# Performance work log

Hardware: AMD Instinct MI355X
Metric: run time of the kernel (lower is better)

Reference implementation:

```python
import jax, jax.numpy as jnp
import numpy as np

N_MODULES = 8
AG_HIDDEN = 512
N_HID = 512
OUT_SIZE = 10
BATCH = 8192


def _state_mask(n_modules, n0, n1):
    # torch: eye(M).repeat_interleave(n0, 0).repeat_interleave(n1, 1)
    m = jnp.eye(n_modules, dtype=jnp.float32)
    return jnp.repeat(jnp.repeat(m, n0, axis=0), n1, axis=1)


def setup_inputs() -> dict:
    key = jax.random.key(0)
    ks = jax.random.split(key, 5)
    d_in = N_MODULES * AG_HIDDEN
    d_hid = N_MODULES * N_HID
    d_out = N_MODULES * OUT_SIZE
    s1 = 1.0 / np.sqrt(d_in)
    s2 = 1.0 / np.sqrt(d_hid)
    return {
        "x": jax.random.normal(ks[0], (BATCH, d_in), jnp.float32),
        "W1": jax.random.uniform(ks[1], (d_hid, d_in), jnp.float32, -s1, s1),
        "b1": jax.random.uniform(ks[2], (d_hid,), jnp.float32, -s1, s1),
        "W2": jax.random.uniform(ks[3], (d_out, d_hid), jnp.float32, -s2, s2),
        "b2": jax.random.uniform(ks[4], (d_out,), jnp.float32, -s2, s2),
    }


def reference(x, W1, b1, W2, b2):
    # block-diagonal masks (intra-module connectivity only)
    mask1 = _state_mask(N_MODULES, N_HID, AG_HIDDEN)   # [d_hid, d_in]
    mask2 = _state_mask(N_MODULES, OUT_SIZE, N_HID)    # [d_out, d_hid]
    h = jax.nn.relu(x @ (W1 * mask1).T + b1)           # [B, d_hid]
    y = h @ (W2 * mask2).T + b2                        # [B, d_out]
    # split(OUT_SIZE, -1) then stack on dim 1 == reshape to [B, n_modules, OUT_SIZE]
    return y.reshape(y.shape[0], N_MODULES, OUT_SIZE)
```

## Files before the change

### kernel.cpp

```cpp
#include <hip/hip_runtime.h>


#define NMOD 8
#define DIM 512
#define OSZ 10
#define BATCH 8192
#define D_IN 4096
#define D_OUT 80
#define BM 128
#define BK 32

typedef __attribute__((ext_vector_type(8))) short short8;
typedef __attribute__((ext_vector_type(4))) float float4v;

__device__ __forceinline__ unsigned short f2bf(float f) {
    unsigned int u = __builtin_bit_cast(unsigned int, f);
    u += 0x7fffu + ((u >> 16) & 1u);
    return (unsigned short)(u >> 16);
}

__device__ __forceinline__ short8 cvt8(float4 a, float4 b) {
    short8 r;
    r[0] = (short)f2bf(a.x); r[1] = (short)f2bf(a.y); r[2] = (short)f2bf(a.z); r[3] = (short)f2bf(a.w);
    r[4] = (short)f2bf(b.x); r[5] = (short)f2bf(b.y); r[6] = (short)f2bf(b.z); r[7] = (short)f2bf(b.w);
    return r;
}

__global__ void cvt_w_kernel(const float* __restrict__ W1, ushort* __restrict__ w1b) {
    int j = blockIdx.x * 256 + threadIdx.x;
    int mm = j >> 16, rem = j & 65535, r = rem >> 7, c4 = rem & 127;
    float4 v = *(const float4*)(W1 + (size_t)(mm * DIM + r) * D_IN + mm * DIM + c4 * 4);
    *(ushort4*)(w1b + (size_t)mm * DIM * DIM + r * DIM + c4 * 4) =
        make_ushort4(f2bf(v.x), f2bf(v.y), f2bf(v.z), f2bf(v.w));
}

template <bool WPRE>
__global__ __launch_bounds__(512, 2)
void fused_kernel(const float* __restrict__ x, const float* __restrict__ W1,
                  const ushort* __restrict__ w1b, const float* __restrict__ b1,
                  const float* __restrict__ W2, const float* __restrict__ b2,
                  float* __restrict__ out) {
    __shared__ ushort smem[40960];
    ushort* ldsA  = smem;
    ushort* ldsB  = smem + 4096;
    ushort* ldsH  = smem;
    ushort* ldsW2 = smem + 32768;

    const int tid  = threadIdx.x;
    const int wave = tid >> 6;
    const int lane = tid & 63;
    const int r16  = lane & 15;
    const int kq   = lane >> 4;

    const int bid     = blockIdx.x;
    const int m       = bid & 7;
    const int rowBase = (bid >> 3) * BM;

    {
        const int row = tid >> 5;
        const int col = (tid & 31) * 16;
        short8 v0 = {0, 0, 0, 0, 0, 0, 0, 0};
        short8 v1 = {0, 0, 0, 0, 0, 0, 0, 0};
        if (row < OSZ) {
            const float* s = W2 + (size_t)(m * OSZ + row) * D_IN + m * DIM + col;
            v0 = cvt8(*(const float4*)s, *(const float4*)(s + 4));
            v1 = cvt8(*(const float4*)(s + 8), *(const float4*)(s + 12));
        }
        const int sw = (row & 7) << 3;
        *(short8*)(ldsW2 + row * DIM + (col ^ sw))       = v0;
        *(short8*)(ldsW2 + row * DIM + ((col + 8) ^ sw)) = v1;
    }

    const float*  xsrc = x + (size_t)rowBase * D_IN + m * DIM;
    const ushort* w1m  = w1b + (size_t)m * DIM * DIM;
    const float*  w1f  = W1 + (size_t)(m * DIM) * D_IN + m * DIM;

    float4v acc[8][4];
#pragma unroll
    for (int i = 0; i < 8; i++)
#pragma unroll
        for (int j = 0; j < 4; j++) acc[i][j] = (float4v){0.f, 0.f, 0.f, 0.f};

    const int arow = tid >> 2;
    const int akc  = tid & 3;

    for (int kk = 0; kk < DIM / BK; kk++) {
        const int k0 = kk * BK;
        {
            const float* s = xsrc + (size_t)arow * D_IN + k0 + akc * 8;
            *(short8*)(ldsA + arow * BK + akc * 8) = cvt8(*(const float4*)s, *(const float4*)(s + 4));
        }
        if (WPRE) {
#pragma unroll
            for (int r = 0; r < 4; r++) {
                short8 v = *(const short8*)(w1m + (size_t)(r * 128 + arow) * DIM + k0 + akc * 8);
                *(short8*)(ldsB + (r * 128 + arow) * BK + akc * 8) = v;
            }
        } else {
#pragma unroll
            for (int r = 0; r < 4; r++) {
                const float* s = w1f + (size_t)(r * 128 + arow) * D_IN + k0 + akc * 8;
                *(short8*)(ldsB + (r * 128 + arow) * BK + akc * 8) =
                    cvt8(*(const float4*)s, *(const float4*)(s + 4));
            }
        }
        __syncthreads();

        short8 aF[8], bF[4];
#pragma unroll
        for (int mt = 0; mt < 8; mt++)
            aF[mt] = *(const short8*)(ldsA + (mt * 16 + r16) * BK + kq * 8);
#pragma unroll
        for (int nt = 0; nt < 4; nt++)
            bF[nt] = *(const short8*)(ldsB + (wave * 64 + nt * 16 + r16) * BK + kq * 8);
#pragma unroll
        for (int mt = 0; mt < 8; mt++)
#pragma unroll
            for (int nt = 0; nt < 4; nt++)
                acc[mt][nt] = __builtin_amdgcn_mfma_f32_16x16x32_bf16(aF[mt], bF[nt], acc[mt][nt], 0, 0, 0);
        __syncthreads();
    }

    float b1v[4];
#pragma unroll
    for (int nt = 0; nt < 4; nt++)
        b1v[nt] = b1[m * DIM + wave * 64 + nt * 16 + r16];

    for (int hh = 0; hh < 2; hh++) {
#pragma unroll
        for (int mt2 = 0; mt2 < 4; mt2++) {
            const int mt = hh * 4 + mt2;
#pragma unroll
            for (int nt = 0; nt < 4; nt++) {
#pragma unroll
                for (int reg = 0; reg < 4; reg++) {
                    float v = acc[mt][nt][reg] + b1v[nt];
                    v = v > 0.f ? v : 0.f;
                    const int lr  = mt2 * 16 + kq * 4 + reg;
                    const int col = wave * 64 + nt * 16 + r16;
                    ldsH[lr * DIM + (col ^ ((lr & 7) << 3))] = f2bf(v);
                }
            }
        }
        __syncthreads();

        if (wave < 4) {
            float4v acc2 = (float4v){0.f, 0.f, 0.f, 0.f};
            const int hrow = wave * 16 + r16;
            const int hsw  = (hrow & 7) << 3;
            const int wsw  = (r16 & 7) << 3;
#pragma unroll
            for (int kk2 = 0; kk2 < 16; kk2++) {
                const int col = kk2 * 32 + kq * 8;
                short8 ha = *(const short8*)(ldsH + hrow * DIM + (col ^ hsw));
                short8 wb = *(const short8*)(ldsW2 + r16 * DIM + (col ^ wsw));
                acc2 = __builtin_amdgcn_mfma_f32_16x16x32_bf16(ha, wb, acc2, 0, 0, 0);
            }
            if (r16 < OSZ) {
                const float b2v = b2[m * OSZ + r16];
#pragma unroll
                for (int reg = 0; reg < 4; reg++) {
                    const int grow = rowBase + hh * 64 + wave * 16 + kq * 4 + reg;
                    out[(size_t)grow * D_OUT + m * OSZ + r16] = acc2[reg] + b2v;
                }
            }
        }
        __syncthreads();
    }
}

extern "C" void kernel_launch(void* const* d_in, const int* in_sizes, int n_in,
                              void* d_out, int out_size, void* d_ws, size_t ws_size,
                              hipStream_t stream) {
    const float* x  = (const float*)d_in[0];
    const float* W1 = (const float*)d_in[1];
    const float* b1 = (const float*)d_in[2];
    const float* W2 = (const float*)d_in[3];
    const float* b2 = (const float*)d_in[4];
    float* out = (float*)d_out;

    if (ws_size >= (size_t)NMOD * DIM * DIM * sizeof(ushort)) {
        ushort* w1b = (ushort*)d_ws;
        cvt_w_kernel<<<dim3(2048), dim3(256), 0, stream>>>(W1, w1b);
        fused_kernel<true><<<dim3(512), dim3(512), 0, stream>>>(x, W1, w1b, b1, W2, b2, out);
    } else {
        fused_kernel<false><<<dim3(512), dim3(512), 0, stream>>>(x, W1, nullptr, b1, W2, b2, out);
    }
}
```

Before: 263.9 us.

## Split hidden dim across blocks with atomic output accumulation and direct-to-LDS weight loads

Shrinks the block tile to 64 rows by 256 hidden columns with 256 threads, so 2048 blocks run instead of 512. The second GEMM's partial sums from the two hidden halves are combined with atomicAdd into an output that a new kernel pre-fills with b2. W1 tiles are now copied straight into LDS with global_load_lds, and an XOR swizzle is added to the A/B LDS layouts. W2 is read from global memory inside the MFMA loop instead of being staged in LDS. Because x is now loaded by both halves, its global traffic doubles, and the change adds an extra launch plus atomics.

```diff
diff --git a/kernel.cpp b/kernel.cpp
--- a/kernel.cpp
+++ b/kernel.cpp
@@ -7,7 +7,8 @@
 #define BATCH 8192
 #define D_IN 4096
 #define D_OUT 80
-#define BM 128
+#define BM 64
+#define BN 256
 #define BK 32
 
 typedef __attribute__((ext_vector_type(8))) short short8;
@@ -26,6 +27,11 @@
     return r;
 }
 
+__global__ void init_out_kernel(const float* __restrict__ b2, float* __restrict__ out) {
+    int idx = blockIdx.x * 256 + threadIdx.x;
+    out[idx] = b2[idx % D_OUT];
+}
+
 __global__ void cvt_w_kernel(const float* __restrict__ W1, ushort* __restrict__ w1b) {
     int j = blockIdx.x * 256 + threadIdx.x;
     int mm = j >> 16, rem = j & 65535, r = rem >> 7, c4 = rem & 127;
@@ -35,16 +41,15 @@
 }
 
 template <bool WPRE>
-__global__ __launch_bounds__(512, 2)
+__global__ __launch_bounds__(256, 3)
 void fused_kernel(const float* __restrict__ x, const float* __restrict__ W1,
                   const ushort* __restrict__ w1b, const float* __restrict__ b1,
                   const float* __restrict__ W2, const float* __restrict__ b2,
                   float* __restrict__ out) {
-    __shared__ ushort smem[40960];
-    ushort* ldsA  = smem;
-    ushort* ldsB  = smem + 4096;
-    ushort* ldsH  = smem;
-    ushort* ldsW2 = smem + 32768;
+    __shared__ ushort smem[16384];
+    ushort* ldsA = smem;
+    ushort* ldsB = smem + 2048;
+    ushort* ldsH = smem;
 
     const int tid  = threadIdx.x;
     const int wave = tid >> 6;
@@ -54,67 +59,63 @@
 
     const int bid     = blockIdx.x;
     const int m       = bid & 7;
-    const int rowBase = (bid >> 3) * BM;
-
-    {
-        const int row = tid >> 5;
-        const int col = (tid & 31) * 16;
-        short8 v0 = {0, 0, 0, 0, 0, 0, 0, 0};
-        short8 v1 = {0, 0, 0, 0, 0, 0, 0, 0};
-        if (row < OSZ) {
-            const float* s = W2 + (size_t)(m * OSZ + row) * D_IN + m * DIM + col;
-            v0 = cvt8(*(const float4*)s, *(const float4*)(s + 4));
-            v1 = cvt8(*(const float4*)(s + 8), *(const float4*)(s + 12));
-        }
-        const int sw = (row & 7) << 3;
-        *(short8*)(ldsW2 + row * DIM + (col ^ sw))       = v0;
-        *(short8*)(ldsW2 + row * DIM + ((col + 8) ^ sw)) = v1;
-    }
+    const int t2      = bid >> 3;
+    const int half    = t2 & 1;
+    const int rowBase = (t2 >> 1) * BM;
 
     const float*  xsrc = x + (size_t)rowBase * D_IN + m * DIM;
-    const ushort* w1m  = w1b + (size_t)m * DIM * DIM;
-    const float*  w1f  = W1 + (size_t)(m * DIM) * D_IN + m * DIM;
+    const ushort* w1m  = w1b + (size_t)m * DIM * DIM + (size_t)half * BN * DIM;
+    const float*  w1f  = W1 + (size_t)(m * DIM + half * BN) * D_IN + m * DIM;
 
-    float4v acc[8][4];
+    float4v acc[4][4];
 #pragma unroll
-    for (int i = 0; i < 8; i++)
+    for (int i = 0; i < 4; i++)
 #pragma unroll
         for (int j = 0; j < 4; j++) acc[i][j] = (float4v){0.f, 0.f, 0.f, 0.f};
 
-    const int arow = tid >> 2;
-    const int akc  = tid & 3;
+    const int srow = tid >> 2;
+    const int sg   = tid & 3;
 
     for (int kk = 0; kk < DIM / BK; kk++) {
         const int k0 = kk * BK;
         {
-            const float* s = xsrc + (size_t)arow * D_IN + k0 + akc * 8;
-            *(short8*)(ldsA + arow * BK + akc * 8) = cvt8(*(const float4*)s, *(const float4*)(s + 4));
+            const int s = (srow >> 1) & 3;
+            const float* p = xsrc + (size_t)srow * D_IN + k0 + sg * 8;
+            *(short8*)(ldsA + srow * BK + (sg ^ s) * 8) = cvt8(*(const float4*)p, *(const float4*)(p + 4));
         }
         if (WPRE) {
 #pragma unroll
             for (int r = 0; r < 4; r++) {
-                short8 v = *(const short8*)(w1m + (size_t)(r * 128 + arow) * DIM + k0 + akc * 8);
-                *(short8*)(ldsB + (r * 128 + arow) * BK + akc * 8) = v;
+                const int row = r * 64 + srow;
+                const int s   = (row >> 1) & 3;
+                __builtin_amdgcn_global_load_lds(
+                    (const __attribute__((address_space(1))) void*)(w1m + (size_t)row * DIM + k0 + (sg ^ s) * 8),
+                    (__attribute__((address_space(3))) void*)(ldsB + row * BK + sg * 8), 16, 0, 0);
             }
         } else {
 #pragma unroll
             for (int r = 0; r < 4; r++) {
-                const float* s = w1f + (size_t)(r * 128 + arow) * D_IN + k0 + akc * 8;
-                *(short8*)(ldsB + (r * 128 + arow) * BK + akc * 8) =
-                    cvt8(*(const float4*)s, *(const float4*)(s + 4));
+                const int row = r * 64 + srow;
+                const int s   = (row >> 1) & 3;
+                const float* p = w1f + (size_t)row * D_IN + k0 + sg * 8;
+                *(short8*)(ldsB + row * BK + (sg ^ s) * 8) = cvt8(*(const float4*)p, *(const float4*)(p + 4));
             }
         }
         __syncthreads();
 
-        short8 aF[8], bF[4];
+        short8 aF[4], bF[4];
 #pragma unroll
-        for (int mt = 0; mt < 8; mt++)
-            aF[mt] = *(const short8*)(ldsA + (mt * 16 + r16) * BK + kq * 8);
+        for (int mt = 0; mt < 4; mt++) {
+            const int row = mt * 16 + r16;
+            aF[mt] = *(const short8*)(ldsA + row * BK + (kq ^ ((row >> 1) & 3)) * 8);
+        }
 #pragma unroll
-        for (int nt = 0; nt < 4; nt++)
-            bF[nt] = *(const short8*)(ldsB + (wave * 64 + nt * 16 + r16) * BK + kq * 8);
+        for (int nt = 0; nt < 4; nt++) {
+            const int row = wave * 64 + nt * 16 + r16;
+            bF[nt] = *(const short8*)(ldsB + row * BK + (kq ^ ((row >> 1) & 3)) * 8);
+        }
 #pragma unroll
-        for (int mt = 0; mt < 8; mt++)
+        for (int mt = 0; mt < 4; mt++)
 #pragma unroll
             for (int nt = 0; nt < 4; nt++)
                 acc[mt][nt] = __builtin_amdgcn_mfma_f32_16x16x32_bf16(aF[mt], bF[nt], acc[mt][nt], 0, 0, 0);
@@ -124,48 +125,47 @@
     float b1v[4];
 #pragma unroll
     for (int nt = 0; nt < 4; nt++)
-        b1v[nt] = b1[m * DIM + wave * 64 + nt * 16 + r16];
+        b1v[nt] = b1[m * DIM + half * BN + wave * 64 + nt * 16 + r16];
 
-    for (int hh = 0; hh < 2; hh++) {
 #pragma unroll
-        for (int mt2 = 0; mt2 < 4; mt2++) {
-            const int mt = hh * 4 + mt2;
+    for (int mt = 0; mt < 4; mt++) {
 #pragma unroll
-            for (int nt = 0; nt < 4; nt++) {
+        for (int nt = 0; nt < 4; nt++) {
 #pragma unroll
-                for (int reg = 0; reg < 4; reg++) {
-                    float v = acc[mt][nt][reg] + b1v[nt];
-                    v = v > 0.f ? v : 0.f;
-                    const int lr  = mt2 * 16 + kq * 4 + reg;
-                    const int col = wave * 64 + nt * 16 + r16;
-                    ldsH[lr * DIM + (col ^ ((lr & 7) << 3))] = f2bf(v);
-                }
+            for (int reg = 0; reg < 4; reg++) {
+                float v = acc[mt][nt][reg] + b1v[nt];
+                v = v > 0.f ? v : 0.f;
+                const int lr  = mt * 16 + kq * 4 + reg;
+                const int col = wave * 64 + nt * 16 + r16;
+                ldsH[lr * BN + (col ^ ((lr & 7) << 3))] = f2bf(v);
             }
         }
-        __syncthreads();
+    }
+    __syncthreads();
 
-        if (wave < 4) {
-            float4v acc2 = (float4v){0.f, 0.f, 0.f, 0.f};
-            const int hrow = wave * 16 + r16;
-            const int hsw  = (hrow & 7) << 3;
-            const int wsw  = (r16 & 7) << 3;
+    {
+        float4v acc2 = (float4v){0.f, 0.f, 0.f, 0.f};
+        const int hrow = wave * 16 + r16;
+        const int hsw  = (hrow & 7) << 3;
+        const float* w2row = W2 + (size_t)(m * OSZ + r16) * D_IN + m * DIM + half * BN;
 #pragma unroll
-            for (int kk2 = 0; kk2 < 16; kk2++) {
-                const int col = kk2 * 32 + kq * 8;
-                short8 ha = *(const short8*)(ldsH + hrow * DIM + (col ^ hsw));
-                short8 wb = *(const short8*)(ldsW2 + r16 * DIM + (col ^ wsw));
-                acc2 = __builtin_amdgcn_mfma_f32_16x16x32_bf16(ha, wb, acc2, 0, 0, 0);
+        for (int kk2 = 0; kk2 < BN / 32; kk2++) {
+            const int c = kk2 * 32 + kq * 8;
+            short8 ha = *(const short8*)(ldsH + hrow * BN + (c ^ hsw));
+            short8 wb = {0, 0, 0, 0, 0, 0, 0, 0};
+            if (r16 < OSZ) {
+                const float* p = w2row + c;
+                wb = cvt8(*(const float4*)p, *(const float4*)(p + 4));
             }
-            if (r16 < OSZ) {
-                const float b2v = b2[m * OSZ + r16];
+            acc2 = __builtin_amdgcn_mfma_f32_16x16x32_bf16(ha, wb, acc2, 0, 0, 0);
+        }
+        if (r16 < OSZ) {
 #pragma unroll
-                for (int reg = 0; reg < 4; reg++) {
-                    const int grow = rowBase + hh * 64 + wave * 16 + kq * 4 + reg;
-                    out[(size_t)grow * D_OUT + m * OSZ + r16] = acc2[reg] + b2v;
-                }
+            for (int reg = 0; reg < 4; reg++) {
+                const int grow = rowBase + wave * 16 + kq * 4 + reg;
+                atomicAdd(out + (size_t)grow * D_OUT + m * OSZ + r16, acc2[reg]);
             }
         }
-        __syncthreads();
     }
 }
 
@@ -179,11 +179,13 @@
     const float* b2 = (const float*)d_in[4];
     float* out = (float*)d_out;
 
+    init_out_kernel<<<dim3(2560), dim3(256), 0, stream>>>(b2, out);
+
     if (ws_size >= (size_t)NMOD * DIM * DIM * sizeof(ushort)) {
         ushort* w1b = (ushort*)d_ws;
         cvt_w_kernel<<<dim3(2048), dim3(256), 0, stream>>>(W1, w1b);
-        fused_kernel<true><<<dim3(512), dim3(512), 0, stream>>>(x, W1, w1b, b1, W2, b2, out);
+        fused_kernel<true><<<dim3(2048), dim3(256), 0, stream>>>(x, W1, w1b, b1, W2, b2, out);
     } else {
-        fused_kernel<false><<<dim3(512), dim3(512), 0, stream>>>(x, W1, nullptr, b1, W2, b2, out);
+        fused_kernel<false><<<dim3(2048), dim3(256), 0, stream>>>(x, W1, nullptr, b1, W2, b2, out);
     }
 }
```

Result: slower. 269.6 us (+2.2%).
